# Performance work log

Hardware: AMD Instinct MI355X
Metric: run time of the kernel (lower is better)

## Reference

```python
import jax, jax.numpy as jnp
import numpy as np

N, NFEAT, NHID, NCLASS, NHEADS = 8192, 512, 64, 16, 4
ALPHA = 0.2          # leaky_relu slope for attention scores
OUT_SLOPE = 0.01     # flax default slope for per-head output leaky_relu
NEG = -9000000000000000.0


def glorot(key, shape):
    fan_in, fan_out = shape[0], shape[1]
    lim = jnp.sqrt(6.0 / (fan_in + fan_out))
    return jax.random.uniform(key, shape, jnp.float32, -lim, lim)


def setup_inputs() -> dict:
    key = jax.random.key(0)
    ks = jax.random.split(key, 6)
    x = jax.random.normal(ks[0], (N, NFEAT), jnp.float32)
    adj = jax.random.randint(ks[1], (N, N), 0, 2, jnp.int32)
    Wh = glorot(ks[2], (NHEADS * NFEAT, NHID)).reshape(NHEADS, NFEAT, NHID)
    ah = glorot(ks[3], (NHEADS * 2 * NHID, 1)).reshape(NHEADS, 2 * NHID, 1)
    Wo = glorot(ks[4], (NHID * NHEADS, NCLASS))
    ao = glorot(ks[5], (2 * NCLASS, 1))
    return {"x": x, "adj": adj, "Wh": Wh, "ah": ah, "Wo": Wo, "ao": ao}


def _gat_layer(x, adj_mask, W, a, score_slope):
    # h: (N, F)
    h = x @ W
    F = h.shape[1]
    # a_input[i,j] = concat(h_i, h_j); a_input @ a == f1[i] + f2[j]
    f1 = h @ a[:F, 0]   # (N,)
    f2 = h @ a[F:, 0]   # (N,)
    e = jax.nn.leaky_relu(f1[:, None] + f2[None, :], negative_slope=score_slope)
    att = jax.nn.softmax(jnp.where(adj_mask, e, NEG), axis=1)  # (N, N)
    return att @ h  # (N, F)


def reference(x, adj, Wh, ah, Wo, ao):
    adj_mask = adj > 0
    heads = []
    for k in range(NHEADS):  # small fixed structural loop
        hp = _gat_layer(x, adj_mask, Wh[k], ah[k], ALPHA)
        heads.append(jax.nn.leaky_relu(hp, negative_slope=OUT_SLOPE))
    xcat = jnp.concatenate(heads, axis=1)  # (N, NHEADS*NHID)
    # output head: concat=False -> return h_prime directly
    return _gat_layer(xcat, adj_mask, Wo, ao, ALPHA)  # (N, NCLASS)
```

## Files before the change

kernel.cpp:

```cpp
#include <hip/hip_runtime.h>
#include <stdint.h>

#define N      8192
#define FEAT   512
#define HID    64
#define NH     4
#define C1     256
#define NCLS   16
#define IPB    8
#define LOG2E  1.44269504f

typedef __attribute__((ext_vector_type(8))) short bf16x8;
typedef __attribute__((ext_vector_type(4))) float f32x4;

__device__ __forceinline__ float b2f(uint16_t u){
  uint32_t x = ((uint32_t)u) << 16;
  return __builtin_bit_cast(float, x);
}
__device__ __forceinline__ uint16_t f2b(float f){
  uint32_t x = __builtin_bit_cast(uint32_t, f);
  uint32_t r = (x + 0x7fffu + ((x >> 16) & 1u)) >> 16;
  return (uint16_t)r;
}
__device__ __forceinline__ float lrelu(float v, float a){ return fmaxf(v, a * v); }
__device__ __forceinline__ float fexp2(float x){
#if __has_builtin(__builtin_amdgcn_exp2f)
  return __builtin_amdgcn_exp2f(x);
#else
  return exp2f(x);
#endif
}
__device__ __forceinline__ uint32_t pk_bf16(float lo, float hi){
  uint32_t r;
  asm("v_cvt_pk_bf16_f32 %0, %1, %2" : "=v"(r) : "v"(lo), "v"(hi));
  return r;
}

__device__ __forceinline__ bf16x8 mk_frag(float f1v, float4 fa, float4 fb,
                                          uint32_t ub, float& dsum){
  float e0, e1, e2, e3, e4, e5, e6, e7, s;
  s = f1v + fa.x; e0 = fexp2(fmaxf(s, 0.2f * s)); if (!(ub &   1u)) e0 = 0.f;
  s = f1v + fa.y; e1 = fexp2(fmaxf(s, 0.2f * s)); if (!(ub &   2u)) e1 = 0.f;
  s = f1v + fa.z; e2 = fexp2(fmaxf(s, 0.2f * s)); if (!(ub &   4u)) e2 = 0.f;
  s = f1v + fa.w; e3 = fexp2(fmaxf(s, 0.2f * s)); if (!(ub &   8u)) e3 = 0.f;
  s = f1v + fb.x; e4 = fexp2(fmaxf(s, 0.2f * s)); if (!(ub &  16u)) e4 = 0.f;
  s = f1v + fb.y; e5 = fexp2(fmaxf(s, 0.2f * s)); if (!(ub &  32u)) e5 = 0.f;
  s = f1v + fb.z; e6 = fexp2(fmaxf(s, 0.2f * s)); if (!(ub &  64u)) e6 = 0.f;
  s = f1v + fb.w; e7 = fexp2(fmaxf(s, 0.2f * s)); if (!(ub & 128u)) e7 = 0.f;
  dsum += ((e0 + e1) + (e2 + e3)) + ((e4 + e5) + (e6 + e7));
  union { uint32_t u[4]; bf16x8 v; } r;
  r.u[0] = pk_bf16(e0, e1);
  r.u[1] = pk_bf16(e2, e3);
  r.u[2] = pk_bf16(e4, e5);
  r.u[3] = pk_bf16(e6, e7);
  return r.v;
}

#define MFMA16(a, b, c) __builtin_amdgcn_mfma_f32_16x16x32_bf16((a), (b), (c), 0, 0, 0)

__global__ __launch_bounds__(256) void kp_pack(const int* __restrict__ adj,
                                               uint32_t* __restrict__ adjT){
  __shared__ uint32_t tile[2][64];
  int t = threadIdx.x, lane = t & 63, wv = t >> 6;
  int jt = blockIdx.x & 127;
  int i0 = (blockIdx.x >> 7) * 64;
  const int j0 = jt * 64;
  #pragma unroll
  for (int r = 0; r < 16; ++r){
    int row = wv * 16 + r;
    unsigned long long mb = __ballot(adj[(size_t)(i0 + row) * N + j0 + lane] > 0);
    if (lane == 0){
      tile[0][row] = (uint32_t)mb;
      tile[1][row] = (uint32_t)(mb >> 32);
    }
  }
  __syncthreads();
  if (t < 128){
    int ww = t >> 6, r = t & 63;
    adjT[(size_t)(jt * 2 + ww) * N + i0 + r] = tile[ww][r];
  }
}

__global__ __launch_bounds__(256) void k1_h(const float* __restrict__ x,
    const float* __restrict__ Wh, const float* __restrict__ ah,
    uint16_t* __restrict__ H, float* __restrict__ f1, float* __restrict__ f2)
{
  int t = threadIdx.x;
  int i0 = blockIdx.x * IPB;
  int k = t >> 6, cc = t & 63;
  const float* wcol = Wh + k * 32768 + cc;
  float acc[IPB] = {};
  for (int f = 0; f < FEAT; f += 4){
    float w0 = wcol[(f + 0) * 64];
    float w1 = wcol[(f + 1) * 64];
    float w2 = wcol[(f + 2) * 64];
    float w3 = wcol[(f + 3) * 64];
    #pragma unroll
    for (int ii = 0; ii < IPB; ++ii){
      const float* xr = x + (size_t)(i0 + ii) * FEAT + f;
      acc[ii] += xr[0] * w0 + xr[1] * w1 + xr[2] * w2 + xr[3] * w3;
    }
  }
  float a1 = ah[k * 128 + cc], a2 = ah[k * 128 + 64 + cc];
  #pragma unroll
  for (int ii = 0; ii < IPB; ++ii){
    int i = i0 + ii;
    H[(size_t)i * C1 + t] = f2b(acc[ii]);
    float c1v = acc[ii] * a1, c2v = acc[ii] * a2;
    #pragma unroll
    for (int off = 32; off; off >>= 1){
      c1v += __shfl_down(c1v, off);
      c2v += __shfl_down(c2v, off);
    }
    if (cc == 0){ f1[k * N + i] = c1v * LOG2E; f2[k * N + i] = c2v * LOG2E; }
  }
}

__global__ void k2a_pack(const uint16_t* __restrict__ H, uint16_t* __restrict__ Bp){
  __shared__ uint16_t tile[64][72];
  int bid = blockIdx.x;
  int k = bid & 3, it = bid >> 2;
  int i0 = it * 64;
  int t = threadIdx.x;
  #pragma unroll
  for (int r = 0; r < 4; ++r){
    int ii = r * 16 + (t >> 4);
    int pp = (t & 15) * 4;
    uint2 v = *(const uint2*)(H + (size_t)(i0 + ii) * C1 + k * 64 + pp);
    const uint16_t* s = (const uint16_t*)&v;
    tile[pp + 0][ii] = s[0]; tile[pp + 1][ii] = s[1];
    tile[pp + 2][ii] = s[2]; tile[pp + 3][ii] = s[3];
  }
  __syncthreads();
  #pragma unroll
  for (int r = 0; r < 2; ++r){
    int jl = r;
    int ct = t >> 6;
    int lane = t & 63;
    int m = lane & 15, q = lane >> 4;
    uint4 v = *(const uint4*)&tile[ct * 16 + m][jl * 32 + q * 8];
    size_t off = ((((size_t)k * 256 + (i0 >> 5) + jl) * 4 + ct) * 64 + lane) * 8;
    *(uint4*)(Bp + off) = v;
  }
}

__global__ __launch_bounds__(1024, 8) void k3_attA(const uint32_t* __restrict__ adjT,
    const uint16_t* __restrict__ Bp, const float* __restrict__ f1,
    const float* __restrict__ f2, uint16_t* __restrict__ xcat)
{
  __shared__ float red[3][4][64][17];
  __shared__ float zred[4][4][16];
  __shared__ float zfin[4][16];

  const int t = threadIdx.x;
  const int gi0 = blockIdx.x * 16;
  const int lane = t & 63;
  const int wv = t >> 6;
  const int head = wv & 3;
  const int jq = wv >> 2;
  const int m = lane & 15;
  const int q = lane >> 4;

  const float* f2js = f2 + (size_t)head * N + jq * 2048;
  const float f1v = f1[(size_t)head * N + gi0 + m];
  const uint16_t* bpbase = Bp + (((size_t)head * 256 + jq * 64) * 4) * 512 + (size_t)lane * 8;
  const uint32_t* aw = adjT + (size_t)(jq * 64) * N + gi0 + m;

  f32x4 acc[4] = {};
  float dsum = 0.f;

  for (int jc = 0; jc < 64; ++jc){
    bf16x8 b[4];
    #pragma unroll
    for (int ct = 0; ct < 4; ++ct)
      b[ct] = *(const bf16x8*)(bpbase + (size_t)(jc * 4 + ct) * 512);
    uint32_t wb = aw[(size_t)jc * N];
    float4 fa = *(const float4*)(f2js + jc * 32 + 8 * q);
    float4 fb = *(const float4*)(f2js + jc * 32 + 8 * q + 4);
    bf16x8 af = mk_frag(f1v, fa, fb, (wb >> (8 * q)) & 255u, dsum);
    #pragma unroll
    for (int ct = 0; ct < 4; ++ct)
      acc[ct] = MFMA16(af, b[ct], acc[ct]);
  }

  dsum += __shfl_xor(dsum, 16);
  dsum += __shfl_xor(dsum, 32);
  if (q == 0) zred[jq][head][m] = dsum;
  if (jq != 0){
    #pragma unroll
    for (int ct = 0; ct < 4; ++ct)
      #pragma unroll
      for (int reg = 0; reg < 4; ++reg)
        red[jq - 1][head][lane][ct * 4 + reg] = acc[ct][reg];
  }
  __syncthreads();
  if (t < 64){
    int h = t >> 4, r = t & 15;
    zfin[h][r] = ((zred[0][h][r] + zred[1][h][r]) + (zred[2][h][r] + zred[3][h][r]));
  }
  __syncthreads();
  if (jq == 0){
    float zv[4];
    #pragma unroll
    for (int reg = 0; reg < 4; ++reg) zv[reg] = zfin[head][q * 4 + reg];
    #pragma unroll
    for (int ct = 0; ct < 4; ++ct)
      #pragma unroll
      for (int reg = 0; reg < 4; ++reg){
        float v = acc[ct][reg] + red[0][head][lane][ct * 4 + reg]
                + red[1][head][lane][ct * 4 + reg] + red[2][head][lane][ct * 4 + reg];
        float r2 = v / zv[reg];
        xcat[(size_t)(gi0 + q * 4 + reg) * C1 + head * 64 + ct * 16 + m] = f2b(lrelu(r2, 0.01f));
      }
  }
}

__global__ __launch_bounds__(256) void k5_h2(const uint16_t* __restrict__ xcat,
    const float* __restrict__ Wo, const float* __restrict__ ao,
    uint16_t* __restrict__ Bp2, float* __restrict__ f1o, float* __restrict__ f2o)
{
  __shared__ uint16_t xs[16][256];
  __shared__ uint16_t hs[16][16];
  int t = threadIdx.x;
  int i0 = blockIdx.x * 16;
  #pragma unroll
  for (int r = 0; r < 2; ++r){
    int idx = t + 256 * r;
    int ii = idx >> 5, o4 = idx & 31;
    *(uint4*)&xs[ii][o4 * 8] = *(const uint4*)(xcat + (size_t)(i0 + ii) * C1 + o4 * 8);
  }
  __syncthreads();
  int ii = t >> 4, c = t & 15;
  float acc = 0.f;
  for (int f = 0; f < 256; ++f)
    acc += b2f(xs[ii][f]) * Wo[f * 16 + c];
  int i = i0 + ii;
  hs[ii][c] = f2b(acc);
  float u1 = acc * ao[c];
  float u2 = acc * ao[16 + c];
  #pragma unroll
  for (int off = 8; off; off >>= 1){
    u1 += __shfl_down(u1, off, 16);
    u2 += __shfl_down(u2, off, 16);
  }
  if (c == 0){ f1o[i] = u1 * LOG2E; f2o[i] = u2 * LOG2E; }
  __syncthreads();
  if (t < 32){
    int q_l = t >> 4, mm = t & 15;
    uint16_t tmp[8];
    #pragma unroll
    for (int s = 0; s < 8; ++s) tmp[s] = hs[8 * q_l + s][mm];
    int jcg = i0 >> 5, half = (i0 >> 4) & 1;
    size_t off = ((size_t)jcg * 64 + (2 * half + q_l) * 16 + mm) * 8;
    *(uint4*)(Bp2 + off) = *(uint4*)tmp;
  }
}

__global__ __launch_bounds__(1024, 8) void k6_attB(const uint32_t* __restrict__ adjT,
    const uint16_t* __restrict__ Bp2, const float* __restrict__ f1o,
    const float* __restrict__ f2o, float* __restrict__ out)
{
  __shared__ float red[15][64][5];
  __shared__ float zredB[16][16];

  const int t = threadIdx.x;
  const int gi0 = blockIdx.x * 16;
  const int lane = t & 63;
  const int wv = t >> 6;
  const int m = lane & 15;
  const int q = lane >> 4;

  const float f1v = f1o[gi0 + m];
  const uint16_t* bp2 = Bp2 + (size_t)(wv * 16) * 512 + (size_t)lane * 8;
  const uint32_t* aw = adjT + (size_t)(wv * 16) * N + gi0 + m;
  const float* f2js = f2o + wv * 512;

  f32x4 acc = {0.f, 0.f, 0.f, 0.f};
  float dsum = 0.f;

  for (int jc = 0; jc < 16; ++jc){
    bf16x8 b = *(const bf16x8*)(bp2 + (size_t)jc * 512);
    uint32_t wb = aw[(size_t)jc * N];
    float4 fa = *(const float4*)(f2js + jc * 32 + 8 * q);
    float4 fb = *(const float4*)(f2js + jc * 32 + 8 * q + 4);
    bf16x8 af = mk_frag(f1v, fa, fb, (wb >> (8 * q)) & 255u, dsum);
    acc = MFMA16(af, b, acc);
  }

  dsum += __shfl_xor(dsum, 16);
  dsum += __shfl_xor(dsum, 32);
  if (q == 0) zredB[wv][m] = dsum;
  if (wv != 0){
    #pragma unroll
    for (int reg = 0; reg < 4; ++reg) red[wv - 1][lane][reg] = acc[reg];
  }
  __syncthreads();
  if (wv == 0){
    float zv[4];
    #pragma unroll
    for (int reg = 0; reg < 4; ++reg){
      float z = 0.f;
      #pragma unroll
      for (int k2 = 0; k2 < 16; ++k2) z += zredB[k2][q * 4 + reg];
      zv[reg] = z;
    }
    #pragma unroll
    for (int reg = 0; reg < 4; ++reg){
      float v = acc[reg];
      #pragma unroll
      for (int k2 = 0; k2 < 15; ++k2) v += red[k2][lane][reg];
      out[(size_t)(gi0 + q * 4 + reg) * NCLS + m] = v / zv[reg];
    }
  }
}

extern "C" void kernel_launch(void* const* d_in, const int* in_sizes, int n_in,
                              void* d_out, int out_size, void* d_ws, size_t ws_size,
                              hipStream_t stream)
{
  const float* x   = (const float*)d_in[0];
  const int*   adj = (const int*)d_in[1];
  const float* Wh  = (const float*)d_in[2];
  const float* ah  = (const float*)d_in[3];
  const float* Wo  = (const float*)d_in[4];
  const float* ao  = (const float*)d_in[5];
  float* out = (float*)d_out;

  char* ws = (char*)d_ws;
  uint16_t* H    = (uint16_t*)(ws);
  uint16_t* Bp   = (uint16_t*)(ws + 4194304);
  float*    f1   = (float*)   (ws + 8388608);
  float*    f2   = (float*)   (ws + 8519680);
  uint16_t* xcat = (uint16_t*)(ws + 8650752);
  uint16_t* Bp2  = (uint16_t*)(ws + 12845056);
  float*    f1o  = (float*)   (ws + 13107200);
  float*    f2o  = (float*)   (ws + 13139968);
  uint32_t* adjT = (uint32_t*)(ws + 13172736);

  hipLaunchKernelGGL(kp_pack,  dim3(16384), dim3(256),  0, stream, adj, adjT);
  hipLaunchKernelGGL(k1_h,     dim3(1024),  dim3(256),  0, stream, x, Wh, ah, H, f1, f2);
  hipLaunchKernelGGL(k2a_pack, dim3(512),   dim3(256),  0, stream, H, Bp);
  hipLaunchKernelGGL(k3_attA,  dim3(512),   dim3(1024), 0, stream, adjT, Bp, f1, f2, xcat);
  hipLaunchKernelGGL(k5_h2,    dim3(512),   dim3(256),  0, stream, xcat, Wo, ao, Bp2, f1o, f2o);
  hipLaunchKernelGGL(k6_attB,  dim3(512),   dim3(1024), 0, stream, adjT, Bp2, f1o, f2o, out);
}
```

Measured before the change: 636.1 us.

## Reuse B fragments across two row tiles and double-buffer B loads in attention kernels

The first-layer attention kernel now gives each block 32 rows and 2 heads, not 16 rows and 4 heads. Each wave builds two A fragments, one per 16-row tile, and applies both to the same loaded B fragments, which halves B-operand global traffic per MFMA. Both attention kernels move to 512-thread blocks and prefetch the next chunk's B fragments into alternate registers while the current chunk computes. The cost is higher register pressure from doubled accumulators and the prefetch buffers. The output-layer kernel gives each wave twice as many column chunks and shrinks its cross-wave reduction.

```diff
diff --git a/kernel.cpp b/kernel.cpp
--- a/kernel.cpp
+++ b/kernel.cpp
@@ -144,74 +144,104 @@
   }
 }
 
-__global__ __launch_bounds__(1024, 8) void k3_attA(const uint32_t* __restrict__ adjT,
+#define K3_LOADB(BD, JC)                                                        \
+  { const int jb = (JC) & 63;                                                   \
+    _Pragma("unroll")                                                           \
+    for (int ct = 0; ct < 4; ++ct)                                              \
+      BD[ct] = *(const bf16x8*)(bpbase + (size_t)(jb * 4 + ct) * 512); }
+
+#define K3_BODY(JC, CUR, NXT)                                                   \
+  {                                                                             \
+    K3_LOADB(b##NXT, (JC) + 1)                                                  \
+    uint32_t wb0 = aw[(size_t)(JC) * N];                                        \
+    uint32_t wb1 = aw[(size_t)(JC) * N + 16];                                   \
+    float4 fa = *(const float4*)(f2js + (JC) * 32 + 8 * q);                     \
+    float4 fb = *(const float4*)(f2js + (JC) * 32 + 8 * q + 4);                 \
+    bf16x8 af0 = mk_frag(f1v0, fa, fb, (wb0 >> (8 * q)) & 255u, dsum0);         \
+    bf16x8 af1 = mk_frag(f1v1, fa, fb, (wb1 >> (8 * q)) & 255u, dsum1);         \
+    _Pragma("unroll")                                                           \
+    for (int ct = 0; ct < 4; ++ct){                                             \
+      acc[0][ct] = MFMA16(af0, b##CUR[ct], acc[0][ct]);                         \
+      acc[1][ct] = MFMA16(af1, b##CUR[ct], acc[1][ct]);                         \
+    }                                                                           \
+  }
+
+__global__ __launch_bounds__(512, 4) void k3_attA(const uint32_t* __restrict__ adjT,
     const uint16_t* __restrict__ Bp, const float* __restrict__ f1,
     const float* __restrict__ f2, uint16_t* __restrict__ xcat)
 {
-  __shared__ float red[3][4][64][17];
-  __shared__ float zred[4][4][16];
-  __shared__ float zfin[4][16];
+  __shared__ float red[3][2][64][33];
+  __shared__ float zred[4][2][2][16];
+  __shared__ float zfin[2][2][16];
 
   const int t = threadIdx.x;
-  const int gi0 = blockIdx.x * 16;
+  const int tile = blockIdx.x >> 1;
+  const int hp   = blockIdx.x & 1;
+  const int gi0  = tile * 32;
+
   const int lane = t & 63;
-  const int wv = t >> 6;
-  const int head = wv & 3;
-  const int jq = wv >> 2;
-  const int m = lane & 15;
-  const int q = lane >> 4;
+  const int wv   = t >> 6;
+  const int hl   = wv & 1;
+  const int jq   = wv >> 1;
+  const int head = hp * 2 + hl;
+  const int m    = lane & 15;
+  const int q    = lane >> 4;
 
   const float* f2js = f2 + (size_t)head * N + jq * 2048;
-  const float f1v = f1[(size_t)head * N + gi0 + m];
-  const uint16_t* bpbase = Bp + (((size_t)head * 256 + jq * 64) * 4) * 512 + (size_t)lane * 8;
+  const float f1v0 = f1[(size_t)head * N + gi0 + m];
+  const float f1v1 = f1[(size_t)head * N + gi0 + 16 + m];
+  const uint16_t* bpbase = Bp + ((size_t)(head * 256 + jq * 64) * 4) * 512 + (size_t)lane * 8;
   const uint32_t* aw = adjT + (size_t)(jq * 64) * N + gi0 + m;
 
-  f32x4 acc[4] = {};
-  float dsum = 0.f;
-
-  for (int jc = 0; jc < 64; ++jc){
-    bf16x8 b[4];
-    #pragma unroll
-    for (int ct = 0; ct < 4; ++ct)
-      b[ct] = *(const bf16x8*)(bpbase + (size_t)(jc * 4 + ct) * 512);
-    uint32_t wb = aw[(size_t)jc * N];
-    float4 fa = *(const float4*)(f2js + jc * 32 + 8 * q);
-    float4 fb = *(const float4*)(f2js + jc * 32 + 8 * q + 4);
-    bf16x8 af = mk_frag(f1v, fa, fb, (wb >> (8 * q)) & 255u, dsum);
-    #pragma unroll
-    for (int ct = 0; ct < 4; ++ct)
-      acc[ct] = MFMA16(af, b[ct], acc[ct]);
-  }
-
-  dsum += __shfl_xor(dsum, 16);
-  dsum += __shfl_xor(dsum, 32);
-  if (q == 0) zred[jq][head][m] = dsum;
+  f32x4 acc[2][4] = {};
+  float dsum0 = 0.f, dsum1 = 0.f;
+
+  bf16x8 bA[4], bB[4];
+  K3_LOADB(bA, 0)
+
+  for (int jc = 0; jc < 64; jc += 2){
+    K3_BODY(jc,     A, B)
+    K3_BODY(jc + 1, B, A)
+  }
+
+  dsum0 += __shfl_xor(dsum0, 16); dsum0 += __shfl_xor(dsum0, 32);
+  dsum1 += __shfl_xor(dsum1, 16); dsum1 += __shfl_xor(dsum1, 32);
+  if (q == 0){ zred[jq][hl][0][m] = dsum0; zred[jq][hl][1][m] = dsum1; }
   if (jq != 0){
     #pragma unroll
-    for (int ct = 0; ct < 4; ++ct)
-      #pragma unroll
-      for (int reg = 0; reg < 4; ++reg)
-        red[jq - 1][head][lane][ct * 4 + reg] = acc[ct][reg];
+    for (int itl = 0; itl < 2; ++itl)
+      #pragma unroll
+      for (int ct = 0; ct < 4; ++ct)
+        #pragma unroll
+        for (int reg = 0; reg < 4; ++reg)
+          red[jq - 1][hl][lane][itl * 16 + ct * 4 + reg] = acc[itl][ct][reg];
   }
   __syncthreads();
   if (t < 64){
-    int h = t >> 4, r = t & 15;
-    zfin[h][r] = ((zred[0][h][r] + zred[1][h][r]) + (zred[2][h][r] + zred[3][h][r]));
+    int h2 = t >> 5, itl2 = (t >> 4) & 1, mm = t & 15;
+    zfin[h2][itl2][mm] = (zred[0][h2][itl2][mm] + zred[1][h2][itl2][mm])
+                       + (zred[2][h2][itl2][mm] + zred[3][h2][itl2][mm]);
   }
   __syncthreads();
   if (jq == 0){
-    float zv[4];
-    #pragma unroll
-    for (int reg = 0; reg < 4; ++reg) zv[reg] = zfin[head][q * 4 + reg];
-    #pragma unroll
-    for (int ct = 0; ct < 4; ++ct)
-      #pragma unroll
-      for (int reg = 0; reg < 4; ++reg){
-        float v = acc[ct][reg] + red[0][head][lane][ct * 4 + reg]
-                + red[1][head][lane][ct * 4 + reg] + red[2][head][lane][ct * 4 + reg];
-        float r2 = v / zv[reg];
-        xcat[(size_t)(gi0 + q * 4 + reg) * C1 + head * 64 + ct * 16 + m] = f2b(lrelu(r2, 0.01f));
-      }
+    #pragma unroll
+    for (int itl = 0; itl < 2; ++itl){
+      float zv[4];
+      #pragma unroll
+      for (int reg = 0; reg < 4; ++reg) zv[reg] = zfin[hl][itl][q * 4 + reg];
+      #pragma unroll
+      for (int ct = 0; ct < 4; ++ct)
+        #pragma unroll
+        for (int reg = 0; reg < 4; ++reg){
+          float v = acc[itl][ct][reg]
+                  + red[0][hl][lane][itl * 16 + ct * 4 + reg]
+                  + red[1][hl][lane][itl * 16 + ct * 4 + reg]
+                  + red[2][hl][lane][itl * 16 + ct * 4 + reg];
+          float r2 = v / zv[reg];
+          xcat[(size_t)(gi0 + itl * 16 + q * 4 + reg) * C1 + head * 64 + ct * 16 + m]
+              = f2b(lrelu(r2, 0.01f));
+        }
+    }
   }
 }
 
@@ -256,12 +286,22 @@
   }
 }
 
-__global__ __launch_bounds__(1024, 8) void k6_attB(const uint32_t* __restrict__ adjT,
+#define K6_BODY(JC, CUR, NXT)                                                   \
+  {                                                                             \
+    b##NXT = *(const bf16x8*)(bp2 + (size_t)(((JC) + 1) & 31) * 512);           \
+    uint32_t wb = aw[(size_t)(JC) * N];                                         \
+    float4 fa = *(const float4*)(f2js + (JC) * 32 + 8 * q);                     \
+    float4 fb = *(const float4*)(f2js + (JC) * 32 + 8 * q + 4);                 \
+    bf16x8 af = mk_frag(f1v, fa, fb, (wb >> (8 * q)) & 255u, dsum);             \
+    acc = MFMA16(af, b##CUR, acc);                                              \
+  }
+
+__global__ __launch_bounds__(512, 4) void k6_attB(const uint32_t* __restrict__ adjT,
     const uint16_t* __restrict__ Bp2, const float* __restrict__ f1o,
     const float* __restrict__ f2o, float* __restrict__ out)
 {
-  __shared__ float red[15][64][5];
-  __shared__ float zredB[16][16];
+  __shared__ float red[7][64][5];
+  __shared__ float zredB[8][16];
 
   const int t = threadIdx.x;
   const int gi0 = blockIdx.x * 16;
@@ -271,20 +311,19 @@
   const int q = lane >> 4;
 
   const float f1v = f1o[gi0 + m];
-  const uint16_t* bp2 = Bp2 + (size_t)(wv * 16) * 512 + (size_t)lane * 8;
-  const uint32_t* aw = adjT + (size_t)(wv * 16) * N + gi0 + m;
-  const float* f2js = f2o + wv * 512;
+  const uint16_t* bp2 = Bp2 + (size_t)(wv * 32) * 512 + (size_t)lane * 8;
+  const uint32_t* aw = adjT + (size_t)(wv * 32) * N + gi0 + m;
+  const float* f2js = f2o + wv * 1024;
 
   f32x4 acc = {0.f, 0.f, 0.f, 0.f};
   float dsum = 0.f;
 
-  for (int jc = 0; jc < 16; ++jc){
-    bf16x8 b = *(const bf16x8*)(bp2 + (size_t)jc * 512);
-    uint32_t wb = aw[(size_t)jc * N];
-    float4 fa = *(const float4*)(f2js + jc * 32 + 8 * q);
-    float4 fb = *(const float4*)(f2js + jc * 32 + 8 * q + 4);
-    bf16x8 af = mk_frag(f1v, fa, fb, (wb >> (8 * q)) & 255u, dsum);
-    acc = MFMA16(af, b, acc);
+  bf16x8 bA, bB;
+  bA = *(const bf16x8*)(bp2);
+
+  for (int jc = 0; jc < 32; jc += 2){
+    K6_BODY(jc,     A, B)
+    K6_BODY(jc + 1, B, A)
   }
 
   dsum += __shfl_xor(dsum, 16);
@@ -296,20 +335,15 @@
   }
   __syncthreads();
   if (wv == 0){
-    float zv[4];
     #pragma unroll
     for (int reg = 0; reg < 4; ++reg){
       float z = 0.f;
       #pragma unroll
-      for (int k2 = 0; k2 < 16; ++k2) z += zredB[k2][q * 4 + reg];
-      zv[reg] = z;
-    }
-    #pragma unroll
-    for (int reg = 0; reg < 4; ++reg){
+      for (int k2 = 0; k2 < 8; ++k2) z += zredB[k2][q * 4 + reg];
       float v = acc[reg];
       #pragma unroll
-      for (int k2 = 0; k2 < 15; ++k2) v += red[k2][lane][reg];
-      out[(size_t)(gi0 + q * 4 + reg) * NCLS + m] = v / zv[reg];
+      for (int k2 = 0; k2 < 7; ++k2) v += red[k2][lane][reg];
+      out[(size_t)(gi0 + q * 4 + reg) * NCLS + m] = v / z;
     }
   }
 }
@@ -337,10 +371,10 @@
   float*    f2o  = (float*)   (ws + 13139968);
   uint32_t* adjT = (uint32_t*)(ws + 13172736);
 
-  hipLaunchKernelGGL(kp_pack,  dim3(16384), dim3(256),  0, stream, adj, adjT);
-  hipLaunchKernelGGL(k1_h,     dim3(1024),  dim3(256),  0, stream, x, Wh, ah, H, f1, f2);
-  hipLaunchKernelGGL(k2a_pack, dim3(512),   dim3(256),  0, stream, H, Bp);
-  hipLaunchKernelGGL(k3_attA,  dim3(512),   dim3(1024), 0, stream, adjT, Bp, f1, f2, xcat);
-  hipLaunchKernelGGL(k5_h2,    dim3(512),   dim3(256),  0, stream, xcat, Wo, ao, Bp2, f1o, f2o);
-  hipLaunchKernelGGL(k6_attB,  dim3(512),   dim3(1024), 0, stream, adjT, Bp2, f1o, f2o, out);
-}
+  hipLaunchKernelGGL(kp_pack,  dim3(16384), dim3(256), 0, stream, adj, adjT);
+  hipLaunchKernelGGL(k1_h,     dim3(1024),  dim3(256), 0, stream, x, Wh, ah, H, f1, f2);
+  hipLaunchKernelGGL(k2a_pack, dim3(512),   dim3(256), 0, stream, H, Bp);
+  hipLaunchKernelGGL(k3_attA,  dim3(512),   dim3(512), 0, stream, adjT, Bp, f1, f2, xcat);
+  hipLaunchKernelGGL(k5_h2,    dim3(512),   dim3(256), 0, stream, xcat, Wo, ao, Bp2, f1o, f2o);
+  hipLaunchKernelGGL(k6_attB,  dim3(512),   dim3(512), 0, stream, adjT, Bp2, f1o, f2o, out);
+}
```

Result: faster. 622.5 us (-2.1%).
